# Performance work log

Hardware: AMD Instinct MI355X
Metric: run time of the kernel (lower is better)

Reference implementation:

```python
import jax, jax.numpy as jnp
import numpy as np
import math

D_MODEL = 1024
N_HEADS = 16
D_K = D_MODEL // N_HEADS


def setup_inputs() -> dict:
    key = jax.random.key(0)
    ks = jax.random.split(key, 12)
    B, S, D = 2, 2048, D_MODEL
    inp = {
        'q': jax.random.normal(ks[0], (B, S, D), jnp.float32),
        'k': jax.random.normal(ks[1], (B, S, D), jnp.float32),
        'v': jax.random.normal(ks[2], (B, S, D), jnp.float32),
        'mask': jnp.ones((B, 1, 1, S), jnp.int32),
    }
    sc = 1.0 / math.sqrt(D)
    inp['wq_w'] = jax.random.normal(ks[3], (D, D), jnp.float32) * sc
    inp['wq_b'] = jnp.zeros((D,), jnp.float32)
    inp['wk_w'] = jax.random.normal(ks[4], (D, D), jnp.float32) * sc
    inp['wk_b'] = jnp.zeros((D,), jnp.float32)
    inp['wv_w'] = jax.random.normal(ks[5], (D, D), jnp.float32) * sc
    inp['wv_b'] = jnp.zeros((D,), jnp.float32)
    inp['wo_w'] = jax.random.normal(ks[6], (D, D), jnp.float32) * sc
    inp['wo_b'] = jnp.zeros((D,), jnp.float32)
    return inp


def reference(q, k, v, mask, wq_w, wq_b, wk_w, wk_b, wv_w, wv_b, wo_w, wo_b):
    B, S, D = q.shape
    H, Dk = N_HEADS, D_K
    scale = math.sqrt(Dk)
    # projections; weights stored as (out, in) like torch Linear -> x @ W^T + b
    def proj(x, w, b):
        y = jnp.einsum('bsd,ed->bse', x, w) + b
        return y.reshape(B, S, H, Dk).transpose(0, 2, 1, 3)  # (B,H,S,Dk)
    qh = proj(q, wq_w, wq_b)
    kh = proj(k, wk_w, wk_b)
    vh = proj(v, wv_w, wv_b)
    scores = jnp.einsum('bhqd,bhkd->bhqk', qh, kh) / scale  # (B,H,S,S)
    scores = jnp.where(mask == 0, jnp.float32(-1e9), scores)
    attention = jax.nn.softmax(scores, axis=-1)
    # dropout is identity at inference (eval mode)
    out = jnp.einsum('bhqk,bhkd->bhqd', attention, vh)  # (B,H,S,Dk)
    out = out.transpose(0, 2, 1, 3).reshape(B, S, D)
    out = jnp.einsum('bsd,ed->bse', out, wo_w) + wo_b
    return out, attention
```

## Files before the change

### kernel.cpp

```cpp
#include <hip/hip_runtime.h>
#include <stdint.h>

#define SB 2048
#define DM 1024
#define NHH 16
#define DKK 64

typedef unsigned short u16;
using short8  = __attribute__((ext_vector_type(8))) short;
using short4v = __attribute__((ext_vector_type(4))) short;
using f32x4   = __attribute__((ext_vector_type(4))) float;

__device__ __forceinline__ u16 f2bf(float f) {
    union { float f; unsigned u; } v; v.f = f;
    unsigned u = v.u;
    return (u16)((u + 0x7FFFu + ((u >> 16) & 1u)) >> 16);
}

__device__ __forceinline__ void stage16(const float* __restrict__ src, u16* dst) {
    const float4* s4 = (const float4*)src;
#pragma unroll
    for (int t = 0; t < 2; ++t) {
        const float4 a = s4[2 * t], b = s4[2 * t + 1];
        short8 p;
        p[0] = (short)f2bf(a.x); p[1] = (short)f2bf(a.y);
        p[2] = (short)f2bf(a.z); p[3] = (short)f2bf(a.w);
        p[4] = (short)f2bf(b.x); p[5] = (short)f2bf(b.y);
        p[6] = (short)f2bf(b.z); p[7] = (short)f2bf(b.w);
        *(short8*)(dst + 8 * t) = p;
    }
}

__global__ __launch_bounds__(256) void proj3_kernel(
    const float* __restrict__ q, const float* __restrict__ k, const float* __restrict__ v,
    const float* __restrict__ wq, const float* __restrict__ bq,
    const float* __restrict__ wk, const float* __restrict__ bk,
    const float* __restrict__ wv, const float* __restrict__ bv,
    u16* __restrict__ qh, u16* __restrict__ kh, u16* __restrict__ vt)
{
    __shared__ __align__(16) u16 As[128 * 72];
    __shared__ __align__(16) u16 Bs[128 * 72];

    const int z = blockIdx.z;
    const float* X  = (z == 0) ? q  : (z == 1) ? k  : v;
    const float* W  = (z == 0) ? wq : (z == 1) ? wk : wv;
    const float* Bv = (z == 0) ? bq : (z == 1) ? bk : bv;
    u16*         Y  = (z == 0) ? qh : (z == 1) ? kh : vt;
    const int vmode = (z == 2);

    const int tid  = threadIdx.x;
    const int lane = tid & 63, wv_ = tid >> 6;
    const int li = lane & 15, g = lane >> 4;
    const int wr = wv_ >> 1, wc = wv_ & 1;
    const int m0 = blockIdx.y * 128, n0 = blockIdx.x * 128;

    f32x4 acc[4][4] = {};

    const int rs = tid >> 2;
    const int cs = (tid & 3) * 16;

    for (int k0 = 0; k0 < DM; k0 += 64) {
        stage16(&X[(m0 + rs) * DM + k0 + cs],      &As[rs * 72 + cs]);
        stage16(&X[(m0 + 64 + rs) * DM + k0 + cs], &As[(64 + rs) * 72 + cs]);
        stage16(&W[(n0 + rs) * DM + k0 + cs],      &Bs[rs * 72 + cs]);
        stage16(&W[(n0 + 64 + rs) * DM + k0 + cs], &Bs[(64 + rs) * 72 + cs]);
        __syncthreads();
#pragma unroll
        for (int kk = 0; kk < 2; ++kk) {
            short8 a[4], b[4];
#pragma unroll
            for (int i = 0; i < 4; ++i)
                a[i] = *(const short8*)&As[(wr * 64 + i * 16 + li) * 72 + kk * 32 + g * 8];
#pragma unroll
            for (int j = 0; j < 4; ++j)
                b[j] = *(const short8*)&Bs[(wc * 64 + j * 16 + li) * 72 + kk * 32 + g * 8];
#pragma unroll
            for (int i = 0; i < 4; ++i)
#pragma unroll
                for (int j = 0; j < 4; ++j)
                    acc[i][j] = __builtin_amdgcn_mfma_f32_16x16x32_bf16(a[i], b[j], acc[i][j], 0, 0, 0);
        }
        __syncthreads();
    }

#pragma unroll
    for (int i = 0; i < 4; ++i)
#pragma unroll
        for (int j = 0; j < 4; ++j) {
            const int n = n0 + wc * 64 + j * 16 + li;
            const float bvv = Bv[n];
            const int mbase = m0 + wr * 64 + i * 16 + g * 4;
            const int h = n >> 6, dk = n & 63;
            if (vmode == 0) {
#pragma unroll
                for (int r = 0; r < 4; ++r) {
                    const int m = mbase + r;
                    const int b = m >> 11, s = m & 2047;
                    Y[(((b * NHH + h) * SB) + s) * DKK + dk] = f2bf(acc[i][j][r] + bvv);
                }
            } else {
                const int b = mbase >> 11, s = mbase & 2047;
                short4v pk;
                pk.x = (short)f2bf(acc[i][j][0] + bvv);
                pk.y = (short)f2bf(acc[i][j][1] + bvv);
                pk.z = (short)f2bf(acc[i][j][2] + bvv);
                pk.w = (short)f2bf(acc[i][j][3] + bvv);
                *(short4v*)&Y[(((b * NHH + h) * DKK) + dk) * SB + s] = pk;
            }
        }
}

__global__ __launch_bounds__(256) void attn_pv_kernel(
    const u16* __restrict__ qh, const u16* __restrict__ kh,
    const u16* __restrict__ vt, const int* __restrict__ mask,
    float* __restrict__ attn_out, u16* __restrict__ oh)
{
    __shared__ __align__(16) u16 Ps[4][32 * 40];
    __shared__ float sl[4][32];
    __shared__ __align__(16) float comb[32 * 68];

    const int tid = threadIdx.x, lane = tid & 63, w = tid >> 6;
    const int li = lane & 15, g = lane >> 4;
    const int bh = blockIdx.y;
    const int q0 = blockIdx.x * 32;
    const int b  = bh >> 4;
    const float sc2 = 0.125f * 1.44269504088896f;

    short8 qa[2][2];
#pragma unroll
    for (int qs = 0; qs < 2; ++qs)
#pragma unroll
        for (int kk = 0; kk < 2; ++kk)
            qa[qs][kk] = *(const short8*)&qh[((bh * SB) + q0 + qs * 16 + li) * DKK + kk * 32 + g * 8];

    float lloc[2][4];
#pragma unroll
    for (int qs = 0; qs < 2; ++qs)
#pragma unroll
        for (int r = 0; r < 4; ++r) lloc[qs][r] = 0.f;

    const int kbase = w * 512;

    for (int kt = 0; kt < 32; ++kt) {
        const int key0 = kbase + kt * 16;
        const short8 kb0 = *(const short8*)&kh[((bh * SB) + key0 + li) * DKK + g * 8];
        const short8 kb1 = *(const short8*)&kh[((bh * SB) + key0 + li) * DKK + 32 + g * 8];
        const int mv = mask[b * SB + key0 + li];
#pragma unroll
        for (int qs = 0; qs < 2; ++qs) {
            f32x4 acc = {};
            acc = __builtin_amdgcn_mfma_f32_16x16x32_bf16(qa[qs][0], kb0, acc, 0, 0, 0);
            acc = __builtin_amdgcn_mfma_f32_16x16x32_bf16(qa[qs][1], kb1, acc, 0, 0, 0);
#pragma unroll
            for (int r = 0; r < 4; ++r) {
                const float s2 = (mv == 0) ? -1.0e9f : fminf(acc[r] * sc2, 80.0f);
                lloc[qs][r] += exp2f(s2);
            }
        }
    }
#pragma unroll
    for (int qs = 0; qs < 2; ++qs)
#pragma unroll
        for (int r = 0; r < 4; ++r) {
            float l = lloc[qs][r];
#pragma unroll
            for (int xm = 1; xm < 16; xm <<= 1) l += __shfl_xor(l, xm);
            lloc[qs][r] = l;
        }
    if (li == 0) {
#pragma unroll
        for (int qs = 0; qs < 2; ++qs)
#pragma unroll
            for (int r = 0; r < 4; ++r)
                sl[w][qs * 16 + g * 4 + r] = lloc[qs][r];
    }
    for (int t = tid; t < 32 * 68; t += 256) comb[t] = 0.f;
    __syncthreads();

    float Li[2][4], Pf[2][4];
#pragma unroll
    for (int qs = 0; qs < 2; ++qs)
#pragma unroll
        for (int r = 0; r < 4; ++r) {
            const int rr = qs * 16 + g * 4 + r;
            const float L = sl[0][rr] + sl[1][rr] + sl[2][rr] + sl[3][rr];
            const bool ok = (L > 1e-37f);
            Li[qs][r] = ok ? 1.0f / L : 0.0f;
            Pf[qs][r] = ok ? 0.0f : (1.0f / 2048.0f);
        }

    f32x4 oacc[2][4] = {};

    for (int pt = 0; pt < 16; ++pt) {
        const int pk0 = kbase + pt * 32;

        short8 vb[4];
#pragma unroll
        for (int jt = 0; jt < 4; ++jt)
            vb[jt] = *(const short8*)&vt[((bh * DKK) + jt * 16 + li) * SB + pk0 + g * 8];

#pragma unroll
        for (int kk2 = 0; kk2 < 2; ++kk2) {
            const int key0 = pk0 + kk2 * 16;
            const short8 kb0 = *(const short8*)&kh[((bh * SB) + key0 + li) * DKK + g * 8];
            const short8 kb1 = *(const short8*)&kh[((bh * SB) + key0 + li) * DKK + 32 + g * 8];
            const int mv = mask[b * SB + key0 + li];
#pragma unroll
            for (int qs = 0; qs < 2; ++qs) {
                f32x4 acc = {};
                acc = __builtin_amdgcn_mfma_f32_16x16x32_bf16(qa[qs][0], kb0, acc, 0, 0, 0);
                acc = __builtin_amdgcn_mfma_f32_16x16x32_bf16(qa[qs][1], kb1, acc, 0, 0, 0);
#pragma unroll
                for (int r = 0; r < 4; ++r) {
                    const float s2 = (mv == 0) ? -1.0e9f : fminf(acc[r] * sc2, 80.0f);
                    const float p = exp2f(s2) * Li[qs][r] + Pf[qs][r];
                    const int row = qs * 16 + g * 4 + r;
                    attn_out[((size_t)(bh * SB + q0 + row)) * SB + key0 + li] = p;
                    Ps[w][row * 40 + kk2 * 16 + li] = f2bf(p);
                }
            }
        }

#pragma unroll
        for (int qs = 0; qs < 2; ++qs) {
            const short8 pa = *(const short8*)&Ps[w][(qs * 16 + li) * 40 + g * 8];
#pragma unroll
            for (int jt = 0; jt < 4; ++jt)
                oacc[qs][jt] = __builtin_amdgcn_mfma_f32_16x16x32_bf16(pa, vb[jt], oacc[qs][jt], 0, 0, 0);
        }
    }

#pragma unroll
    for (int qs = 0; qs < 2; ++qs)
#pragma unroll
        for (int jt = 0; jt < 4; ++jt)
#pragma unroll
            for (int r = 0; r < 4; ++r)
                atomicAdd(&comb[(qs * 16 + g * 4 + r) * 68 + jt * 16 + li], oacc[qs][jt][r]);
    __syncthreads();

    {
        const int row = tid >> 3, c0 = (tid & 7) * 8;
        short8 pk;
#pragma unroll
        for (int j = 0; j < 8; ++j) pk[j] = (short)f2bf(comb[row * 68 + c0 + j]);
        *(short8*)&oh[((bh * SB) + q0 + row) * DKK + c0] = pk;
    }
}

__global__ __launch_bounds__(256) void oproj_kernel(
    const u16* __restrict__ OH, const float* __restrict__ W,
    const float* __restrict__ Bv, float* __restrict__ Y)
{
    __shared__ __align__(16) u16 As[128 * 72];
    __shared__ __align__(16) u16 Bs[128 * 72];

    const int tid  = threadIdx.x;
    const int lane = tid & 63, wv = tid >> 6;
    const int li = lane & 15, g = lane >> 4;
    const int wr = wv >> 1, wc = wv & 1;
    const int m0 = blockIdx.y * 128, n0 = blockIdx.x * 128;

    f32x4 acc[4][4] = {};
    const int rs = tid >> 2;
    const int cs = (tid & 3) * 16;
    const int r0 = tid >> 3;
    const int c0 = (tid & 7) * 8;

    for (int k0 = 0; k0 < DM; k0 += 64) {
        const int h = k0 >> 6;
#pragma unroll
        for (int rr = 0; rr < 4; ++rr) {
            const int m = m0 + rr * 32 + r0, bb = m >> 11, s = m & 2047;
            *(short8*)&As[(rr * 32 + r0) * 72 + c0] =
                *(const short8*)&OH[(((bb * NHH + h) * SB) + s) * DKK + c0];
        }
        stage16(&W[(n0 + rs) * DM + k0 + cs],      &Bs[rs * 72 + cs]);
        stage16(&W[(n0 + 64 + rs) * DM + k0 + cs], &Bs[(64 + rs) * 72 + cs]);
        __syncthreads();
#pragma unroll
        for (int kk = 0; kk < 2; ++kk) {
            short8 a[4], bq[4];
#pragma unroll
            for (int i = 0; i < 4; ++i)
                a[i] = *(const short8*)&As[(wr * 64 + i * 16 + li) * 72 + kk * 32 + g * 8];
#pragma unroll
            for (int j = 0; j < 4; ++j)
                bq[j] = *(const short8*)&Bs[(wc * 64 + j * 16 + li) * 72 + kk * 32 + g * 8];
#pragma unroll
            for (int i = 0; i < 4; ++i)
#pragma unroll
                for (int j = 0; j < 4; ++j)
                    acc[i][j] = __builtin_amdgcn_mfma_f32_16x16x32_bf16(a[i], bq[j], acc[i][j], 0, 0, 0);
        }
        __syncthreads();
    }

#pragma unroll
    for (int i = 0; i < 4; ++i)
#pragma unroll
        for (int j = 0; j < 4; ++j) {
            const int n = n0 + wc * 64 + j * 16 + li;
            const float bv = Bv[n];
            const int mbase = m0 + wr * 64 + i * 16 + g * 4;
#pragma unroll
            for (int r = 0; r < 4; ++r)
                Y[(mbase + r) * DM + n] = acc[i][j][r] + bv;
        }
}

extern "C" void kernel_launch(void* const* d_in, const int* in_sizes, int n_in,
                              void* d_out, int out_size, void* d_ws, size_t ws_size,
                              hipStream_t stream) {
    const float* q    = (const float*)d_in[0];
    const float* k    = (const float*)d_in[1];
    const float* v    = (const float*)d_in[2];
    const int*   mask = (const int*)d_in[3];
    const float* wq   = (const float*)d_in[4];
    const float* bq   = (const float*)d_in[5];
    const float* wk   = (const float*)d_in[6];
    const float* bk   = (const float*)d_in[7];
    const float* wv   = (const float*)d_in[8];
    const float* bv   = (const float*)d_in[9];
    const float* wo   = (const float*)d_in[10];
    const float* bo   = (const float*)d_in[11];

    float* out  = (float*)d_out;
    float* attn = out + 4194304;

    u16* ws = (u16*)d_ws;
    u16* qh = ws;
    u16* kh = ws + 1 * 4194304;
    u16* vt = ws + 2 * 4194304;
    u16* oh = ws;

    dim3 blk(256);
    proj3_kernel<<<dim3(8, 32, 3), blk, 0, stream>>>(q, k, v, wq, bq, wk, bk, wv, bv, qh, kh, vt);
    attn_pv_kernel<<<dim3(64, 32), blk, 0, stream>>>(qh, kh, vt, mask, attn, oh);
    oproj_kernel<<<dim3(8, 32), blk, 0, stream>>>(oh, wo, bo, out);
}
```

Baseline: 906.5 us.

## Give each wave its own 16 query rows over all keys in attention

The attention kernel stops splitting the key range across the four waves, which needed a shared-memory row-sum exchange, two block barriers and LDS atomic accumulation of partial outputs. Now each wave owns 16 query rows and walks all 2048 keys itself, so the row sum is reduced with shuffles alone and the output is written straight from registers. The attention-probability stores become nontemporal, and the grid is halved to 64 query rows per block. In exchange each wave runs a longer serial loop, and the four waves in a block no longer share key or value reads.

```diff
diff --git a/kernel.cpp b/kernel.cpp
--- a/kernel.cpp
+++ b/kernel.cpp
@@ -115,137 +115,94 @@
     const u16* __restrict__ vt, const int* __restrict__ mask,
     float* __restrict__ attn_out, u16* __restrict__ oh)
 {
-    __shared__ __align__(16) u16 Ps[4][32 * 40];
-    __shared__ float sl[4][32];
-    __shared__ __align__(16) float comb[32 * 68];
+    __shared__ __align__(16) u16 Ps[4][16 * 40];
 
     const int tid = threadIdx.x, lane = tid & 63, w = tid >> 6;
     const int li = lane & 15, g = lane >> 4;
     const int bh = blockIdx.y;
-    const int q0 = blockIdx.x * 32;
+    const int q0 = blockIdx.x * 64 + w * 16;
     const int b  = bh >> 4;
     const float sc2 = 0.125f * 1.44269504088896f;
 
-    short8 qa[2][2];
-#pragma unroll
-    for (int qs = 0; qs < 2; ++qs)
-#pragma unroll
-        for (int kk = 0; kk < 2; ++kk)
-            qa[qs][kk] = *(const short8*)&qh[((bh * SB) + q0 + qs * 16 + li) * DKK + kk * 32 + g * 8];
-
-    float lloc[2][4];
-#pragma unroll
-    for (int qs = 0; qs < 2; ++qs)
-#pragma unroll
-        for (int r = 0; r < 4; ++r) lloc[qs][r] = 0.f;
-
-    const int kbase = w * 512;
-
-    for (int kt = 0; kt < 32; ++kt) {
-        const int key0 = kbase + kt * 16;
-        const short8 kb0 = *(const short8*)&kh[((bh * SB) + key0 + li) * DKK + g * 8];
-        const short8 kb1 = *(const short8*)&kh[((bh * SB) + key0 + li) * DKK + 32 + g * 8];
-        const int mv = mask[b * SB + key0 + li];
-#pragma unroll
-        for (int qs = 0; qs < 2; ++qs) {
+    const u16* __restrict__ qhb = qh + (size_t)bh * SB * DKK;
+    const u16* __restrict__ khb = kh + (size_t)bh * SB * DKK;
+    const u16* __restrict__ vtb = vt + (size_t)bh * DKK * SB;
+    const int* __restrict__ mkb = mask + b * SB;
+    float* __restrict__ aob = attn_out + (size_t)bh * SB * SB;
+
+    short8 qa[2];
+#pragma unroll
+    for (int kk = 0; kk < 2; ++kk)
+        qa[kk] = *(const short8*)&qhb[(q0 + li) * DKK + kk * 32 + g * 8];
+
+    float lloc[4] = {0.f, 0.f, 0.f, 0.f};
+
+#pragma unroll 2
+    for (int kt = 0; kt < 128; ++kt) {
+        const int key0 = kt * 16;
+        const short8 kb0 = *(const short8*)&khb[(key0 + li) * DKK + g * 8];
+        const short8 kb1 = *(const short8*)&khb[(key0 + li) * DKK + 32 + g * 8];
+        const int mv = mkb[key0 + li];
+        f32x4 acc = {};
+        acc = __builtin_amdgcn_mfma_f32_16x16x32_bf16(qa[0], kb0, acc, 0, 0, 0);
+        acc = __builtin_amdgcn_mfma_f32_16x16x32_bf16(qa[1], kb1, acc, 0, 0, 0);
+#pragma unroll
+        for (int r = 0; r < 4; ++r) {
+            const float s2 = (mv == 0) ? -1.0e9f : fminf(acc[r] * sc2, 80.0f);
+            lloc[r] += exp2f(s2);
+        }
+    }
+    float Li[4], Pf[4];
+#pragma unroll
+    for (int r = 0; r < 4; ++r) {
+        float l = lloc[r];
+#pragma unroll
+        for (int xm = 1; xm < 16; xm <<= 1) l += __shfl_xor(l, xm);
+        const bool ok = (l > 1e-37f);
+        Li[r] = ok ? 1.0f / l : 0.0f;
+        Pf[r] = ok ? 0.0f : (1.0f / 2048.0f);
+    }
+
+    f32x4 oacc[4] = {};
+
+    for (int pt = 0; pt < 64; ++pt) {
+        const int pk0 = pt * 32;
+
+        short8 vb[4];
+#pragma unroll
+        for (int jt = 0; jt < 4; ++jt)
+            vb[jt] = *(const short8*)&vtb[(jt * 16 + li) * SB + pk0 + g * 8];
+
+#pragma unroll
+        for (int kk2 = 0; kk2 < 2; ++kk2) {
+            const int key0 = pk0 + kk2 * 16;
+            const short8 kb0 = *(const short8*)&khb[(key0 + li) * DKK + g * 8];
+            const short8 kb1 = *(const short8*)&khb[(key0 + li) * DKK + 32 + g * 8];
+            const int mv = mkb[key0 + li];
             f32x4 acc = {};
-            acc = __builtin_amdgcn_mfma_f32_16x16x32_bf16(qa[qs][0], kb0, acc, 0, 0, 0);
-            acc = __builtin_amdgcn_mfma_f32_16x16x32_bf16(qa[qs][1], kb1, acc, 0, 0, 0);
+            acc = __builtin_amdgcn_mfma_f32_16x16x32_bf16(qa[0], kb0, acc, 0, 0, 0);
+            acc = __builtin_amdgcn_mfma_f32_16x16x32_bf16(qa[1], kb1, acc, 0, 0, 0);
 #pragma unroll
             for (int r = 0; r < 4; ++r) {
                 const float s2 = (mv == 0) ? -1.0e9f : fminf(acc[r] * sc2, 80.0f);
-                lloc[qs][r] += exp2f(s2);
+                const float p = exp2f(s2) * Li[r] + Pf[r];
+                const int row = g * 4 + r;
+                __builtin_nontemporal_store(p, &aob[(size_t)(q0 + row) * SB + key0 + li]);
+                Ps[w][row * 40 + kk2 * 16 + li] = f2bf(p);
             }
         }
-    }
-#pragma unroll
-    for (int qs = 0; qs < 2; ++qs)
-#pragma unroll
-        for (int r = 0; r < 4; ++r) {
-            float l = lloc[qs][r];
-#pragma unroll
-            for (int xm = 1; xm < 16; xm <<= 1) l += __shfl_xor(l, xm);
-            lloc[qs][r] = l;
-        }
-    if (li == 0) {
-#pragma unroll
-        for (int qs = 0; qs < 2; ++qs)
-#pragma unroll
-            for (int r = 0; r < 4; ++r)
-                sl[w][qs * 16 + g * 4 + r] = lloc[qs][r];
-    }
-    for (int t = tid; t < 32 * 68; t += 256) comb[t] = 0.f;
-    __syncthreads();
-
-    float Li[2][4], Pf[2][4];
-#pragma unroll
-    for (int qs = 0; qs < 2; ++qs)
-#pragma unroll
-        for (int r = 0; r < 4; ++r) {
-            const int rr = qs * 16 + g * 4 + r;
-            const float L = sl[0][rr] + sl[1][rr] + sl[2][rr] + sl[3][rr];
-            const bool ok = (L > 1e-37f);
-            Li[qs][r] = ok ? 1.0f / L : 0.0f;
-            Pf[qs][r] = ok ? 0.0f : (1.0f / 2048.0f);
-        }
-
-    f32x4 oacc[2][4] = {};
-
-    for (int pt = 0; pt < 16; ++pt) {
-        const int pk0 = kbase + pt * 32;
-
-        short8 vb[4];
+
+        const short8 pa = *(const short8*)&Ps[w][li * 40 + g * 8];
 #pragma unroll
         for (int jt = 0; jt < 4; ++jt)
-            vb[jt] = *(const short8*)&vt[((bh * DKK) + jt * 16 + li) * SB + pk0 + g * 8];
-
-#pragma unroll
-        for (int kk2 = 0; kk2 < 2; ++kk2) {
-            const int key0 = pk0 + kk2 * 16;
-            const short8 kb0 = *(const short8*)&kh[((bh * SB) + key0 + li) * DKK + g * 8];
-            const short8 kb1 = *(const short8*)&kh[((bh * SB) + key0 + li) * DKK + 32 + g * 8];
-            const int mv = mask[b * SB + key0 + li];
-#pragma unroll
-            for (int qs = 0; qs < 2; ++qs) {
-                f32x4 acc = {};
-                acc = __builtin_amdgcn_mfma_f32_16x16x32_bf16(qa[qs][0], kb0, acc, 0, 0, 0);
-                acc = __builtin_amdgcn_mfma_f32_16x16x32_bf16(qa[qs][1], kb1, acc, 0, 0, 0);
-#pragma unroll
-                for (int r = 0; r < 4; ++r) {
-                    const float s2 = (mv == 0) ? -1.0e9f : fminf(acc[r] * sc2, 80.0f);
-                    const float p = exp2f(s2) * Li[qs][r] + Pf[qs][r];
-                    const int row = qs * 16 + g * 4 + r;
-                    attn_out[((size_t)(bh * SB + q0 + row)) * SB + key0 + li] = p;
-                    Ps[w][row * 40 + kk2 * 16 + li] = f2bf(p);
-                }
-            }
-        }
-
-#pragma unroll
-        for (int qs = 0; qs < 2; ++qs) {
-            const short8 pa = *(const short8*)&Ps[w][(qs * 16 + li) * 40 + g * 8];
-#pragma unroll
-            for (int jt = 0; jt < 4; ++jt)
-                oacc[qs][jt] = __builtin_amdgcn_mfma_f32_16x16x32_bf16(pa, vb[jt], oacc[qs][jt], 0, 0, 0);
-        }
-    }
-
-#pragma unroll
-    for (int qs = 0; qs < 2; ++qs)
-#pragma unroll
-        for (int jt = 0; jt < 4; ++jt)
-#pragma unroll
-            for (int r = 0; r < 4; ++r)
-                atomicAdd(&comb[(qs * 16 + g * 4 + r) * 68 + jt * 16 + li], oacc[qs][jt][r]);
-    __syncthreads();
-
-    {
-        const int row = tid >> 3, c0 = (tid & 7) * 8;
-        short8 pk;
-#pragma unroll
-        for (int j = 0; j < 8; ++j) pk[j] = (short)f2bf(comb[row * 68 + c0 + j]);
-        *(short8*)&oh[((bh * SB) + q0 + row) * DKK + c0] = pk;
-    }
+            oacc[jt] = __builtin_amdgcn_mfma_f32_16x16x32_bf16(pa, vb[jt], oacc[jt], 0, 0, 0);
+    }
+
+#pragma unroll
+    for (int jt = 0; jt < 4; ++jt)
+#pragma unroll
+        for (int r = 0; r < 4; ++r)
+            oh[((size_t)bh * SB + q0 + g * 4 + r) * DKK + jt * 16 + li] = f2bf(oacc[jt][r]);
 }
 
 __global__ __launch_bounds__(256) void oproj_kernel(
@@ -336,6 +293,6 @@
 
     dim3 blk(256);
     proj3_kernel<<<dim3(8, 32, 3), blk, 0, stream>>>(q, k, v, wq, bq, wk, bk, wv, bv, qh, kh, vt);
-    attn_pv_kernel<<<dim3(64, 32), blk, 0, stream>>>(qh, kh, vt, mask, attn, oh);
+    attn_pv_kernel<<<dim3(32, 32), blk, 0, stream>>>(qh, kh, vt, mask, attn, oh);
     oproj_kernel<<<dim3(8, 32), blk, 0, stream>>>(oh, wo, bo, out);
 }
```

After: 985.2 us. 8.7% more time.
